# Optimization experiments

Hardware: AMD Instinct MI355X
Metric: run time of the kernel (lower is better)

The kernel has to match this reference:

```python
import jax, jax.numpy as jnp
import numpy as np

M = 41
RHO = M / 2.0          # rho=-1 -> M/2
OVERLAPS = 40
STRIDES = 40
N_FFT = OVERLAPS + STRIDES   # 80
HOP = STRIDES                # 40

def _get_index():
    S = []
    for n1 in range(-(M // 2), M // 2):
        for n2 in range(-(M // 2), M // 2):
            if abs(n1 * n2) <= RHO * (M // 2):
                S.append((n1, n2))
    return np.asarray(S, dtype=np.int64)

IDX = _get_index()          # [K,2], K=1600
N1 = IDX[:, 0]
N2 = IDX[:, 1]
K = len(IDX)

def setup_inputs() -> dict:
    key = jax.random.key(0)
    ks = jax.random.split(key, 7)
    b, L, m = 2, 2080, 2
    return {
        "x_real": jax.random.normal(ks[0], (b, L, m), jnp.float32),
        "x_imag": jax.random.normal(ks[1], (b, L, m), jnp.float32),
        "task_info": jax.random.uniform(ks[2], (b, 4), jnp.float32),
        "w_real": jax.random.normal(ks[3], (K,), jnp.float32) * 0.02,
        "w_imag": jax.random.normal(ks[4], (K,), jnp.float32) * 0.02,
        "b_real": jax.random.normal(ks[5], (1,), jnp.float32) * 0.02,
        "b_imag": jax.random.normal(ks[6], (1,), jnp.float32) * 0.02,
    }

def _stft(x):
    # x: [b, L, m] complex -> [b, T, F, m]; rectangular window, center=False
    L = x.shape[1]
    T = (L - N_FFT) // HOP + 1
    idx = np.arange(T)[:, None] * HOP + np.arange(N_FFT)[None, :]
    frames = x[:, idx, :]                      # [b, T, F, m]
    return jnp.fft.fft(frames, axis=2)

def _istft(X, L):
    # X: [b, T, F, m] -> [b, L, m] via overlap-add, rect-window normalization
    frames = jnp.fft.ifft(X, axis=2)
    b, T, F, m = X.shape
    idx = (np.arange(T)[:, None] * HOP + np.arange(F)[None, :]).reshape(-1)
    y = jnp.zeros((b, L, m), X.dtype).at[:, idx, :].add(frames.reshape(b, -1, m))
    cov = np.zeros(L)
    np.add.at(cov, idx, 1.0)
    cov = jnp.asarray(np.where(cov > 0, cov, 1.0), jnp.float32)
    return y / cov[None, :, None]

def reference(x_real, x_imag, task_info, w_real, w_imag, b_real, b_imag):
    x = x_real + 1j * x_imag                   # [b, L, m] complex64
    b, L, m = x.shape
    # get_power: launch power (dBm in task_info[:,0]) -> mW per mode
    P = jnp.power(10.0, task_info[:, 0] / 10.0) / m   # [b]
    X = _stft(x)                               # [b, T, F, m]
    F = N_FFT
    f = np.arange(F)
    g1 = (f[None, :] - N1[:, None]) % F        # [K, F] : torch.roll(X, n1, dims=2)
    g12 = (f[None, :] - (N1 + N2)[:, None]) % F
    g2 = (f[None, :] - N2[:, None]) % F
    # A_k = roll(X,n1) * conj(roll(X,n1+n2))   -> [b, T, K, F, m]
    A = X[:, :, g1, :] * jnp.conj(X[:, :, g12, :])
    A = A + jnp.roll(A, 1, axis=1)             # + previous frame (circular)
    E = A * X[:, :, g2, :]                     # [b, T, K, F, m]
    w = (w_real + 1j * w_imag).astype(E.dtype)
    bias = (b_real[0] + 1j * b_imag[0]).astype(E.dtype)
    delta = jnp.einsum('btkfm,k->btfm', E, w) + bias   # ComplexLinear(K,1)
    d = _istft(delta, L)                       # [b, L, m]
    out = x + d * P[:, None, None].astype(d.dtype)
    return out[:, OVERLAPS // 2: L - OVERLAPS // 2, :]
```

## Files before the change

kernel.cpp:

```cpp
#include <hip/hip_runtime.h>
#include <math.h>

#define BATCH 2
#define LLEN  2080
#define MCH   2
#define TT    51
#define FF    80
#define HOP   40
#define KW    1600
#define OUTL  2040
#define NT    640
#define NB    (BATCH * TT * MCH)
#define ZROW  161
#define PI_F  3.14159265358979323846f

__global__ __launch_bounds__(NT) void fused_k1(
    const float* __restrict__ xr, const float* __restrict__ xi,
    const float* __restrict__ wr, const float* __restrict__ wi,
    const float* __restrict__ br, const float* __restrict__ bi,
    float2* __restrict__ Fr)
{
    __shared__ float2 xs[2 * FF];
    __shared__ float2 tw[FF];
    __shared__ float2 Yt2[2 * FF];
    __shared__ float2 Yp[FF];
    __shared__ float2 Wsh[KW];
    __shared__ float2 Zall[40][ZROW];
    __shared__ float2 dvec[FF];

    float2* flat = &Zall[0][0];

    int tid = threadIdx.x;
    int bid = blockIdx.x;
    int b   = bid / (TT * MCH);
    int rem = bid % (TT * MCH);
    int t   = rem / MCH;
    int mi  = rem % MCH;
    int tp  = (t + TT - 1) % TT;

    float bre = br[0], bim = bi[0];

    float2 wreg0 = make_float2(wr[tid],        wi[tid]);
    float2 wreg1 = make_float2(wr[tid + NT],   wi[tid + NT]);
    float2 wreg2 = make_float2(0.f, 0.f);
    if (tid < KW - 2 * NT)
        wreg2 = make_float2(wr[tid + 2 * NT], wi[tid + 2 * NT]);

    if (tid < 2 * FF) {
        int frm = tid / FF, j = tid % FF;
        int tt  = (frm == 0) ? t : tp;
        int g = (b * LLEN + tt * HOP + j) * MCH + mi;
        xs[tid] = make_float2(xr[g], xi[g]);
    } else if (tid < 240) {
        int jj = tid - 160;
        float s, c;
        sincosf((2.0f * PI_F / FF) * (float)jj, &s, &c);
        tw[jj] = make_float2(c, s);
    }
    __syncthreads();

    {
        int o    = tid >> 2;
        int pq   = tid & 3;
        int ff   = o % FF;
        int frm  = o / FF;
        const float2* xb = &xs[frm * FF];

        int q = (ff * pq) & 3;
        float2 tv = (q == 0) ? make_float2(1.f, 0.f)
                  : (q == 1) ? make_float2(0.f, -1.f)
                  : (q == 2) ? make_float2(-1.f, 0.f)
                  :            make_float2(0.f, 1.f);
        float sp, cp;
        sincosf(-(2.0f * PI_F / FF) * (float)ff, &sp, &cp);
        float2 st = make_float2(cp, sp);

        float2 a = make_float2(0.f, 0.f);
        int j = pq * 20;
        #pragma unroll 4
        for (int i = 0; i < 20; ++i, ++j) {
            float2 xv = xb[j];
            a.x += xv.x * tv.x - xv.y * tv.y;
            a.y += xv.x * tv.y + xv.y * tv.x;
            float nx = tv.x * st.x - tv.y * st.y;
            tv.y = tv.x * st.y + tv.y * st.x;
            tv.x = nx;
        }
        flat[pq * 160 + o] = a;
    }
    __syncthreads();
    if (tid < 2 * FF) {
        float2 s = make_float2(0.f, 0.f);
        for (int p = 0; p < 4; ++p) {
            float2 v = flat[p * 160 + tid];
            s.x += v.x; s.y += v.y;
        }
        if (tid < FF) {
            Yt2[tid + 20] = s;
            Yt2[(tid < 60) ? (tid + 100) : (tid - 60)] = s;
        } else {
            Yp[tid - FF] = s;
        }
    }
    __syncthreads();

    for (int i = 0; i < 5; ++i) {
        int zi = tid + i * NT;
        int jn = zi / FF;
        int g  = zi % FF;
        int n2 = jn - 20;
        int gm = g - n2; if (gm >= FF) gm -= FF; if (gm < 0) gm += FF;
        float2 a  = Yt2[g + 20], bm = Yt2[gm + 20];
        float2 cc = Yp[g],       dm = Yp[gm];
        float zre = a.x * bm.x + a.y * bm.y + cc.x * dm.x + cc.y * dm.y;
        float zim = a.y * bm.x - a.x * bm.y + cc.y * dm.x - cc.x * dm.y;
        float2 z = make_float2(zre, zim);
        Zall[jn][g + 20] = z;
        Zall[jn][(g < 60) ? (g + 100) : (g - 60)] = z;
    }
    {
        Wsh[tid]      = wreg0;
        Wsh[tid + NT] = wreg1;
        if (tid < KW - 2 * NT) Wsh[tid + 2 * NT] = wreg2;
    }
    __syncthreads();

    float2 o0, o1, o2, o3, o4;
    int jn, fb;
    {
        jn = tid >> 4;
        int fg = tid & 15;
        fb = fg * 5;
        const float2* zz = &Zall[jn][0];

        float2 S0 = make_float2(0.f,0.f), S1 = S0, S2 = S0, S3 = S0, S4 = S0;
        float2 w0 = zz[fb + 40], w1 = zz[fb + 41], w2 = zz[fb + 42],
               w3 = zz[fb + 43], w4 = zz[fb + 44];
        #pragma unroll
        for (int jn1 = 0; jn1 < 40; ++jn1) {
            float2 wv = Wsh[jn1 * 40 + jn];
            S0.x += wv.x * w0.x - wv.y * w0.y;  S0.y += wv.x * w0.y + wv.y * w0.x;
            S1.x += wv.x * w1.x - wv.y * w1.y;  S1.y += wv.x * w1.y + wv.y * w1.x;
            S2.x += wv.x * w2.x - wv.y * w2.y;  S2.y += wv.x * w2.y + wv.y * w2.x;
            S3.x += wv.x * w3.x - wv.y * w3.y;  S3.y += wv.x * w3.y + wv.y * w3.x;
            S4.x += wv.x * w4.x - wv.y * w4.y;  S4.y += wv.x * w4.y + wv.y * w4.x;
            if (jn1 < 39) {
                float2 nv = zz[fb + 39 - jn1];
                w4 = w3; w3 = w2; w2 = w1; w1 = w0; w0 = nv;
            }
        }
        float2 y;
        y = Yt2[fb + 0 - jn + 40]; o0 = make_float2(y.x*S0.x - y.y*S0.y, y.x*S0.y + y.y*S0.x);
        y = Yt2[fb + 1 - jn + 40]; o1 = make_float2(y.x*S1.x - y.y*S1.y, y.x*S1.y + y.y*S1.x);
        y = Yt2[fb + 2 - jn + 40]; o2 = make_float2(y.x*S2.x - y.y*S2.y, y.x*S2.y + y.y*S2.x);
        y = Yt2[fb + 3 - jn + 40]; o3 = make_float2(y.x*S3.x - y.y*S3.y, y.x*S3.y + y.y*S3.x);
        y = Yt2[fb + 4 - jn + 40]; o4 = make_float2(y.x*S4.x - y.y*S4.y, y.x*S4.y + y.y*S4.x);
    }
    __syncthreads();
    flat[jn * FF + fb + 0] = o0;
    flat[jn * FF + fb + 1] = o1;
    flat[jn * FF + fb + 2] = o2;
    flat[jn * FF + fb + 3] = o3;
    flat[jn * FF + fb + 4] = o4;
    __syncthreads();

    {
        int f = tid % FF;
        int p = tid / FF;
        float2 s = make_float2(0.f, 0.f);
        for (int q2 = 0; q2 < 5; ++q2) {
            float2 v = flat[(p * 5 + q2) * FF + f];
            s.x += v.x; s.y += v.y;
        }
        flat[3200 + p * FF + f] = s;
    }
    __syncthreads();
    if (tid < FF) {
        float2 s = make_float2(bre, bim);
        #pragma unroll
        for (int p = 0; p < 8; ++p) {
            float2 v = flat[3200 + p * FF + tid];
            s.x += v.x; s.y += v.y;
        }
        dvec[tid] = s;
    }
    __syncthreads();

    {
        int j  = tid >> 3;
        int p8 = tid & 7;
        float2 a = make_float2(0.f, 0.f);
        int f0 = p8 * 10;
        int r  = (j * f0) % FF;
        #pragma unroll 5
        for (int i = 0; i < 10; ++i) {
            float2 dv = dvec[f0 + i];
            float2 tv = tw[r];
            a.x += dv.x * tv.x - dv.y * tv.y;
            a.y += dv.x * tv.y + dv.y * tv.x;
            r += j; if (r >= FF) r -= FF;
        }
        flat[p8 * FF + j] = a;
    }
    __syncthreads();
    if (tid < FF) {
        float2 s = make_float2(0.f, 0.f);
        #pragma unroll
        for (int p = 0; p < 8; ++p) {
            float2 v = flat[p * FF + tid];
            s.x += v.x; s.y += v.y;
        }
        s.x *= (1.0f / FF);
        s.y *= (1.0f / FF);
        Fr[((b * TT + t) * MCH + mi) * FF + tid] = s;
    }
}

__global__ void out_kernel(
    const float* __restrict__ xr, const float* __restrict__ xi,
    const float* __restrict__ ti, const float2* __restrict__ Fr,
    float* __restrict__ out, int out_size)
{
    int idx = blockIdx.x * blockDim.x + threadIdx.x;
    int tot = BATCH * OUTL * MCH;
    if (idx >= tot) return;
    int mi  = idx % MCH;
    int rem = idx / MCH;
    int lo  = rem % OUTL;
    int b   = rem / OUTL;
    int l   = lo + 20;

    float P = exp2f(ti[b * 4] * 0.33219280948873623f) * 0.5f;

    int t1 = l / HOP;
    int t0 = t1 - 1;
    float2 acc = make_float2(0.f, 0.f);
    float cov = 0.f;
    if (t1 <= TT - 1) {
        float2 v = Fr[((b * TT + t1) * MCH + mi) * FF + (l - HOP * t1)];
        acc.x += v.x; acc.y += v.y; cov += 1.f;
    }
    if (t0 >= 0) {
        float2 v = Fr[((b * TT + t0) * MCH + mi) * FF + (l - HOP * t0)];
        acc.x += v.x; acc.y += v.y; cov += 1.f;
    }
    float inv = 1.0f / cov;
    acc.x *= inv; acc.y *= inv;

    int gi = (b * LLEN + l) * MCH + mi;
    float outr = xr[gi] + acc.x * P;
    if (out_size == tot) {
        out[idx] = outr;
    } else {
        float outi = xi[gi] + acc.y * P;
        out[idx * 2]     = outr;
        out[idx * 2 + 1] = outi;
    }
}

extern "C" void kernel_launch(void* const* d_in, const int* in_sizes, int n_in,
                              void* d_out, int out_size, void* d_ws, size_t ws_size,
                              hipStream_t stream)
{
    const float* xr = (const float*)d_in[0];
    const float* xi = (const float*)d_in[1];
    const float* ti = (const float*)d_in[2];
    const float* wr = (const float*)d_in[3];
    const float* wi = (const float*)d_in[4];
    const float* br = (const float*)d_in[5];
    const float* bi = (const float*)d_in[6];

    float2* Fr = (float2*)d_ws;

    fused_k1<<<NB, NT, 0, stream>>>(xr, xi, wr, wi, br, bi, Fr);

    int tot = BATCH * OUTL * MCH;
    out_kernel<<<(tot + 255) / 256, 256, 0, stream>>>(xr, xi, ti, Fr,
                                                      (float*)d_out, out_size);
}
```

Before: 17.22 us.

## Fuse overlap-add output into single kernel with per-segment duplicate frame work

Merges the two kernels into one. Each block now owns a 40-sample output segment and recomputes both overlapping frames (current and previous), including their DFTs and nonlinear sums, so it can do the overlap-add, normalization and residual write directly. This removes the second launch and the workspace round-trip through global memory. In exchange each block does roughly twice the arithmetic and uses about twice the shared memory, which lowers occupancy. The DFT split is also changed from four partial sums to two, combined with a warp shuffle instead of a shared-memory reduction.

```diff
diff --git a/kernel.cpp b/kernel.cpp
--- a/kernel.cpp
+++ b/kernel.cpp
@@ -10,75 +10,78 @@
 #define KW    1600
 #define OUTL  2040
 #define NT    640
-#define NB    (BATCH * TT * MCH)
+#define NS    52
+#define NB    (BATCH * NS * MCH)
 #define ZROW  161
 #define PI_F  3.14159265358979323846f
 
-__global__ __launch_bounds__(NT) void fused_k1(
+__global__ __launch_bounds__(NT) void mono_kernel(
     const float* __restrict__ xr, const float* __restrict__ xi,
+    const float* __restrict__ ti,
     const float* __restrict__ wr, const float* __restrict__ wi,
     const float* __restrict__ br, const float* __restrict__ bi,
-    float2* __restrict__ Fr)
+    float* __restrict__ out, int out_size)
 {
-    __shared__ float2 xs[2 * FF];
+    __shared__ float2 xs[4 * FF];
     __shared__ float2 tw[FF];
-    __shared__ float2 Yt2[2 * FF];
-    __shared__ float2 Yp[FF];
+    __shared__ float2 Ysh[4][2 * FF];
     __shared__ float2 Wsh[KW];
-    __shared__ float2 Zall[40][ZROW];
-    __shared__ float2 dvec[FF];
-
-    float2* flat = &Zall[0][0];
+    __shared__ float2 Zall[2][40][ZROW];
+    __shared__ float2 dvec[2 * FF];
+
+    float2* flat = &Zall[0][0][0];
 
     int tid = threadIdx.x;
     int bid = blockIdx.x;
-    int b   = bid / (TT * MCH);
-    int rem = bid % (TT * MCH);
-    int t   = rem / MCH;
+    int b   = bid / (NS * MCH);
+    int rem = bid % (NS * MCH);
+    int s   = rem / MCH;
     int mi  = rem % MCH;
-    int tp  = (t + TT - 1) % TT;
+
+    bool dAv = (s <= TT - 1);
+    bool dBv = (s >= 1);
+    int tA  = dAv ? s : 0;
+    int tAp = (tA + TT - 1) % TT;
+    int tB  = dBv ? s - 1 : 0;
+    int tBp = (tB + TT - 1) % TT;
 
     float bre = br[0], bim = bi[0];
 
-    float2 wreg0 = make_float2(wr[tid],        wi[tid]);
-    float2 wreg1 = make_float2(wr[tid + NT],   wi[tid + NT]);
+    float2 wreg0 = make_float2(wr[tid],      wi[tid]);
+    float2 wreg1 = make_float2(wr[tid + NT], wi[tid + NT]);
     float2 wreg2 = make_float2(0.f, 0.f);
     if (tid < KW - 2 * NT)
         wreg2 = make_float2(wr[tid + 2 * NT], wi[tid + 2 * NT]);
 
-    if (tid < 2 * FF) {
-        int frm = tid / FF, j = tid % FF;
-        int tt  = (frm == 0) ? t : tp;
-        int g = (b * LLEN + tt * HOP + j) * MCH + mi;
+    if (tid < 4 * FF) {
+        int slot = tid / FF, j = tid % FF;
+        int tslot = (slot == 0) ? tA : (slot == 1) ? tAp : (slot == 2) ? tB : tBp;
+        int g = (b * LLEN + tslot * HOP + j) * MCH + mi;
         xs[tid] = make_float2(xr[g], xi[g]);
-    } else if (tid < 240) {
-        int jj = tid - 160;
-        float s, c;
-        sincosf((2.0f * PI_F / FF) * (float)jj, &s, &c);
-        tw[jj] = make_float2(c, s);
-    }
-    __syncthreads();
-
-    {
-        int o    = tid >> 2;
-        int pq   = tid & 3;
+    } else if (tid < 4 * FF + FF) {
+        int jj = tid - 4 * FF;
+        float sn, cs;
+        sincosf((2.0f * PI_F / FF) * (float)jj, &sn, &cs);
+        tw[jj] = make_float2(cs, sn);
+    }
+    __syncthreads();
+
+    {
+        int o    = tid >> 1;
+        int pq   = tid & 1;
+        int slot = o / FF;
         int ff   = o % FF;
-        int frm  = o / FF;
-        const float2* xb = &xs[frm * FF];
-
-        int q = (ff * pq) & 3;
-        float2 tv = (q == 0) ? make_float2(1.f, 0.f)
-                  : (q == 1) ? make_float2(0.f, -1.f)
-                  : (q == 2) ? make_float2(-1.f, 0.f)
-                  :            make_float2(0.f, 1.f);
+        const float2* xb = &xs[slot * FF];
+
+        float2 tv = ((ff & pq) & 1) ? make_float2(-1.f, 0.f) : make_float2(1.f, 0.f);
         float sp, cp;
         sincosf(-(2.0f * PI_F / FF) * (float)ff, &sp, &cp);
         float2 st = make_float2(cp, sp);
 
         float2 a = make_float2(0.f, 0.f);
-        int j = pq * 20;
+        int j = pq * 40;
         #pragma unroll 4
-        for (int i = 0; i < 20; ++i, ++j) {
+        for (int i = 0; i < 40; ++i, ++j) {
             float2 xv = xb[j];
             a.x += xv.x * tv.x - xv.y * tv.y;
             a.y += xv.x * tv.y + xv.y * tv.x;
@@ -86,175 +89,161 @@
             tv.y = tv.x * st.y + tv.y * st.x;
             tv.x = nx;
         }
-        flat[pq * 160 + o] = a;
-    }
-    __syncthreads();
-    if (tid < 2 * FF) {
-        float2 s = make_float2(0.f, 0.f);
-        for (int p = 0; p < 4; ++p) {
-            float2 v = flat[p * 160 + tid];
-            s.x += v.x; s.y += v.y;
-        }
-        if (tid < FF) {
-            Yt2[tid + 20] = s;
-            Yt2[(tid < 60) ? (tid + 100) : (tid - 60)] = s;
-        } else {
-            Yp[tid - FF] = s;
-        }
-    }
-    __syncthreads();
-
-    for (int i = 0; i < 5; ++i) {
+        a.x += __shfl_xor(a.x, 1);
+        a.y += __shfl_xor(a.y, 1);
+        if (pq == 0) {
+            Ysh[slot][ff + 20] = a;
+            Ysh[slot][(ff < 60) ? (ff + 100) : (ff - 60)] = a;
+        }
+    }
+    __syncthreads();
+
+    #pragma unroll
+    for (int i = 0; i < 10; ++i) {
         int zi = tid + i * NT;
-        int jn = zi / FF;
-        int g  = zi % FF;
-        int n2 = jn - 20;
-        int gm = g - n2; if (gm >= FF) gm -= FF; if (gm < 0) gm += FF;
-        float2 a  = Yt2[g + 20], bm = Yt2[gm + 20];
-        float2 cc = Yp[g],       dm = Yp[gm];
+        int d  = zi / 3200;
+        int rr = zi % 3200;
+        int jn = rr / FF;
+        int g  = rr % FF;
+        const float2* Ya = Ysh[2 * d];
+        const float2* Yp = Ysh[2 * d + 1];
+        float2 a  = Ya[g + 20], bm = Ya[g - jn + 40];
+        float2 cc = Yp[g + 20], dm = Yp[g - jn + 40];
         float zre = a.x * bm.x + a.y * bm.y + cc.x * dm.x + cc.y * dm.y;
         float zim = a.y * bm.x - a.x * bm.y + cc.y * dm.x - cc.x * dm.y;
         float2 z = make_float2(zre, zim);
-        Zall[jn][g + 20] = z;
-        Zall[jn][(g < 60) ? (g + 100) : (g - 60)] = z;
-    }
-    {
-        Wsh[tid]      = wreg0;
-        Wsh[tid + NT] = wreg1;
-        if (tid < KW - 2 * NT) Wsh[tid + 2 * NT] = wreg2;
-    }
-    __syncthreads();
-
-    float2 o0, o1, o2, o3, o4;
-    int jn, fb;
-    {
-        jn = tid >> 4;
-        int fg = tid & 15;
-        fb = fg * 5;
-        const float2* zz = &Zall[jn][0];
-
-        float2 S0 = make_float2(0.f,0.f), S1 = S0, S2 = S0, S3 = S0, S4 = S0;
-        float2 w0 = zz[fb + 40], w1 = zz[fb + 41], w2 = zz[fb + 42],
-               w3 = zz[fb + 43], w4 = zz[fb + 44];
+        Zall[d][jn][g + 20] = z;
+        Zall[d][jn][(g < 60) ? (g + 100) : (g - 60)] = z;
+    }
+    Wsh[tid]      = wreg0;
+    Wsh[tid + NT] = wreg1;
+    if (tid < KW - 2 * NT) Wsh[tid + 2 * NT] = wreg2;
+    __syncthreads();
+
+    {
+        int d  = tid / 320;
+        int rr = tid % 320;
+        int jn = rr >> 3;
+        int fg = rr & 7;
+        int fb = fg * 10;
+        const float2* zz = &Zall[d][jn][0];
+        const float2* Ya = Ysh[2 * d];
+
+        float2 S[10], W[10];
+        #pragma unroll
+        for (int q = 0; q < 10; ++q) { S[q] = make_float2(0.f, 0.f); W[q] = zz[fb + 40 + q]; }
         #pragma unroll
         for (int jn1 = 0; jn1 < 40; ++jn1) {
             float2 wv = Wsh[jn1 * 40 + jn];
-            S0.x += wv.x * w0.x - wv.y * w0.y;  S0.y += wv.x * w0.y + wv.y * w0.x;
-            S1.x += wv.x * w1.x - wv.y * w1.y;  S1.y += wv.x * w1.y + wv.y * w1.x;
-            S2.x += wv.x * w2.x - wv.y * w2.y;  S2.y += wv.x * w2.y + wv.y * w2.x;
-            S3.x += wv.x * w3.x - wv.y * w3.y;  S3.y += wv.x * w3.y + wv.y * w3.x;
-            S4.x += wv.x * w4.x - wv.y * w4.y;  S4.y += wv.x * w4.y + wv.y * w4.x;
+            #pragma unroll
+            for (int q = 0; q < 10; ++q) {
+                S[q].x += wv.x * W[q].x - wv.y * W[q].y;
+                S[q].y += wv.x * W[q].y + wv.y * W[q].x;
+            }
             if (jn1 < 39) {
-                float2 nv = zz[fb + 39 - jn1];
-                w4 = w3; w3 = w2; w2 = w1; w1 = w0; w0 = nv;
-            }
-        }
-        float2 y;
-        y = Yt2[fb + 0 - jn + 40]; o0 = make_float2(y.x*S0.x - y.y*S0.y, y.x*S0.y + y.y*S0.x);
-        y = Yt2[fb + 1 - jn + 40]; o1 = make_float2(y.x*S1.x - y.y*S1.y, y.x*S1.y + y.y*S1.x);
-        y = Yt2[fb + 2 - jn + 40]; o2 = make_float2(y.x*S2.x - y.y*S2.y, y.x*S2.y + y.y*S2.x);
-        y = Yt2[fb + 3 - jn + 40]; o3 = make_float2(y.x*S3.x - y.y*S3.y, y.x*S3.y + y.y*S3.x);
-        y = Yt2[fb + 4 - jn + 40]; o4 = make_float2(y.x*S4.x - y.y*S4.y, y.x*S4.y + y.y*S4.x);
-    }
-    __syncthreads();
-    flat[jn * FF + fb + 0] = o0;
-    flat[jn * FF + fb + 1] = o1;
-    flat[jn * FF + fb + 2] = o2;
-    flat[jn * FF + fb + 3] = o3;
-    flat[jn * FF + fb + 4] = o4;
-    __syncthreads();
-
-    {
-        int f = tid % FF;
-        int p = tid / FF;
-        float2 s = make_float2(0.f, 0.f);
-        for (int q2 = 0; q2 < 5; ++q2) {
-            float2 v = flat[(p * 5 + q2) * FF + f];
-            s.x += v.x; s.y += v.y;
-        }
-        flat[3200 + p * FF + f] = s;
-    }
-    __syncthreads();
-    if (tid < FF) {
-        float2 s = make_float2(bre, bim);
-        #pragma unroll
-        for (int p = 0; p < 8; ++p) {
-            float2 v = flat[3200 + p * FF + tid];
-            s.x += v.x; s.y += v.y;
-        }
-        dvec[tid] = s;
-    }
-    __syncthreads();
-
-    {
-        int j  = tid >> 3;
-        int p8 = tid & 7;
+                #pragma unroll
+                for (int q = 9; q > 0; --q) W[q] = W[q - 1];
+                W[0] = zz[fb + 39 - jn1];
+            }
+        }
+        float2 O[10];
+        #pragma unroll
+        for (int q = 0; q < 10; ++q) {
+            float2 y = Ya[fb + q - jn + 40];
+            O[q] = make_float2(y.x * S[q].x - y.y * S[q].y,
+                               y.x * S[q].y + y.y * S[q].x);
+        }
+        __syncthreads();
+        #pragma unroll
+        for (int q = 0; q < 10; ++q)
+            flat[d * 3200 + jn * 80 + fb + q] = O[q];
+    }
+    __syncthreads();
+
+    {
+        int d  = tid / 320;
+        int rr = tid % 320;
+        int p  = rr / FF;
+        int f  = rr % FF;
+        float2 sum = make_float2(0.f, 0.f);
+        #pragma unroll
+        for (int q = 0; q < 10; ++q) {
+            float2 v = flat[d * 3200 + (p * 10 + q) * 80 + f];
+            sum.x += v.x; sum.y += v.y;
+        }
+        flat[6400 + d * 320 + p * 80 + f] = sum;
+    }
+    __syncthreads();
+    if (tid < 160) {
+        int d = tid / FF, f = tid % FF;
+        float2 sum = make_float2(bre, bim);
+        #pragma unroll
+        for (int p = 0; p < 4; ++p) {
+            float2 v = flat[6400 + d * 320 + p * 80 + f];
+            sum.x += v.x; sum.y += v.y;
+        }
+        dvec[d * FF + f] = sum;
+    }
+    __syncthreads();
+
+    {
+        int d   = tid / 320;
+        int rr  = tid % 320;
+        int j40 = rr >> 3;
+        int p8  = rr & 7;
+        int j   = j40 + 40 * d;
         float2 a = make_float2(0.f, 0.f);
         int f0 = p8 * 10;
         int r  = (j * f0) % FF;
         #pragma unroll 5
         for (int i = 0; i < 10; ++i) {
-            float2 dv = dvec[f0 + i];
+            float2 dv = dvec[d * FF + f0 + i];
             float2 tv = tw[r];
             a.x += dv.x * tv.x - dv.y * tv.y;
             a.y += dv.x * tv.y + dv.y * tv.x;
             r += j; if (r >= FF) r -= FF;
         }
-        flat[p8 * FF + j] = a;
-    }
-    __syncthreads();
-    if (tid < FF) {
-        float2 s = make_float2(0.f, 0.f);
-        #pragma unroll
-        for (int p = 0; p < 8; ++p) {
-            float2 v = flat[p * FF + tid];
-            s.x += v.x; s.y += v.y;
-        }
-        s.x *= (1.0f / FF);
-        s.y *= (1.0f / FF);
-        Fr[((b * TT + t) * MCH + mi) * FF + tid] = s;
-    }
-}
-
-__global__ void out_kernel(
-    const float* __restrict__ xr, const float* __restrict__ xi,
-    const float* __restrict__ ti, const float2* __restrict__ Fr,
-    float* __restrict__ out, int out_size)
-{
-    int idx = blockIdx.x * blockDim.x + threadIdx.x;
-    int tot = BATCH * OUTL * MCH;
-    if (idx >= tot) return;
-    int mi  = idx % MCH;
-    int rem = idx / MCH;
-    int lo  = rem % OUTL;
-    int b   = rem / OUTL;
-    int l   = lo + 20;
-
-    float P = exp2f(ti[b * 4] * 0.33219280948873623f) * 0.5f;
-
-    int t1 = l / HOP;
-    int t0 = t1 - 1;
-    float2 acc = make_float2(0.f, 0.f);
-    float cov = 0.f;
-    if (t1 <= TT - 1) {
-        float2 v = Fr[((b * TT + t1) * MCH + mi) * FF + (l - HOP * t1)];
-        acc.x += v.x; acc.y += v.y; cov += 1.f;
-    }
-    if (t0 >= 0) {
-        float2 v = Fr[((b * TT + t0) * MCH + mi) * FF + (l - HOP * t0)];
-        acc.x += v.x; acc.y += v.y; cov += 1.f;
-    }
-    float inv = 1.0f / cov;
-    acc.x *= inv; acc.y *= inv;
-
-    int gi = (b * LLEN + l) * MCH + mi;
-    float outr = xr[gi] + acc.x * P;
-    if (out_size == tot) {
-        out[idx] = outr;
-    } else {
-        float outi = xi[gi] + acc.y * P;
-        out[idx * 2]     = outr;
-        out[idx * 2 + 1] = outi;
+        flat[(d * 40 + j40) * 8 + p8] = a;
+    }
+    __syncthreads();
+
+    if (tid < 40) {
+        int j40 = tid;
+        int l = 40 * s + j40;
+        if (l >= 20 && l < LLEN - 20) {
+            float2 acc = make_float2(0.f, 0.f);
+            float cov = 0.f;
+            if (dAv) {
+                #pragma unroll
+                for (int p = 0; p < 8; ++p) {
+                    float2 v = flat[j40 * 8 + p];
+                    acc.x += v.x; acc.y += v.y;
+                }
+                cov += 1.f;
+            }
+            if (dBv) {
+                #pragma unroll
+                for (int p = 0; p < 8; ++p) {
+                    float2 v = flat[(40 + j40) * 8 + p];
+                    acc.x += v.x; acc.y += v.y;
+                }
+                cov += 1.f;
+            }
+            float P   = exp2f(ti[b * 4] * 0.33219280948873623f) * 0.5f;
+            float inv = 1.0f / ((float)FF * cov);
+            float ar = acc.x * inv, ai = acc.y * inv;
+            int gi = (b * LLEN + l) * MCH + mi;
+            int lo = l - 20;
+            int p  = (b * OUTL + lo) * MCH + mi;
+            const int tot = BATCH * OUTL * MCH;
+            float outr = xr[gi] + ar * P;
+            if (out_size == tot) {
+                out[p] = outr;
+            } else {
+                out[p * 2]     = outr;
+                out[p * 2 + 1] = xi[gi] + ai * P;
+            }
+        }
     }
 }
 
@@ -270,11 +259,6 @@
     const float* br = (const float*)d_in[5];
     const float* bi = (const float*)d_in[6];
 
-    float2* Fr = (float2*)d_ws;
-
-    fused_k1<<<NB, NT, 0, stream>>>(xr, xi, wr, wi, br, bi, Fr);
-
-    int tot = BATCH * OUTL * MCH;
-    out_kernel<<<(tot + 255) / 256, 256, 0, stream>>>(xr, xi, ti, Fr,
-                                                      (float*)d_out, out_size);
+    mono_kernel<<<NB, NT, 0, stream>>>(xr, xi, ti, wr, wi, br, bi,
+                                       (float*)d_out, out_size);
 }
```

Result: slower. 21.27 us (+23.5%).

## Split each frame's K-sum across two half-blocks and combine partials in output kernel

Applied to the files above, without the earlier changes.

Each frame/channel block is split into two blocks of 320 threads, each handling half of the n2 index range, which doubles the grid from 204 to 408 blocks and halves shared memory per block. The per-frame DFT now uses a twiddle-table lookup over two partial sums instead of four with on-the-fly rotation. Each half writes its own partial inverse-DFT result to a separate workspace slice, and the output kernel sums the two. The aim is to fill more CUs on the device. In exchange, the forward DFT and the inverse-DFT steps are now computed in both halves, and the output kernel does extra global reads.

```diff
diff --git a/kernel.cpp b/kernel.cpp
--- a/kernel.cpp
+++ b/kernel.cpp
@@ -9,8 +9,9 @@
 #define HOP   40
 #define KW    1600
 #define OUTL  2040
-#define NT    640
-#define NB    (BATCH * TT * MCH)
+#define NT    320
+#define NHB   (BATCH * TT * MCH * 2)
+#define NFR   (BATCH * TT * MCH)
 #define ZROW  161
 #define PI_F  3.14159265358979323846f
 
@@ -18,33 +19,29 @@
     const float* __restrict__ xr, const float* __restrict__ xi,
     const float* __restrict__ wr, const float* __restrict__ wi,
     const float* __restrict__ br, const float* __restrict__ bi,
-    float2* __restrict__ Fr)
+    float2* __restrict__ FrH)
 {
     __shared__ float2 xs[2 * FF];
     __shared__ float2 tw[FF];
     __shared__ float2 Yt2[2 * FF];
     __shared__ float2 Yp[FF];
-    __shared__ float2 Wsh[KW];
-    __shared__ float2 Zall[40][ZROW];
+    __shared__ float2 Wsh[40 * 20];
+    __shared__ float2 Zall[20][ZROW];
     __shared__ float2 dvec[FF];
 
     float2* flat = &Zall[0][0];
 
     int tid = threadIdx.x;
     int bid = blockIdx.x;
-    int b   = bid / (TT * MCH);
-    int rem = bid % (TT * MCH);
+    int h   = bid & 1;
+    int fid = bid >> 1;
+    int b   = fid / (TT * MCH);
+    int rem = fid % (TT * MCH);
     int t   = rem / MCH;
     int mi  = rem % MCH;
     int tp  = (t + TT - 1) % TT;
 
     float bre = br[0], bim = bi[0];
-
-    float2 wreg0 = make_float2(wr[tid],        wi[tid]);
-    float2 wreg1 = make_float2(wr[tid + NT],   wi[tid + NT]);
-    float2 wreg2 = make_float2(0.f, 0.f);
-    if (tid < KW - 2 * NT)
-        wreg2 = make_float2(wr[tid + 2 * NT], wi[tid + 2 * NT]);
 
     if (tid < 2 * FF) {
         int frm = tid / FF, j = tid % FF;
@@ -57,44 +54,36 @@
         sincosf((2.0f * PI_F / FF) * (float)jj, &s, &c);
         tw[jj] = make_float2(c, s);
     }
-    __syncthreads();
-
-    {
-        int o    = tid >> 2;
-        int pq   = tid & 3;
+    for (int k = tid; k < 800; k += NT) {
+        int jn1 = k / 20, jl = k % 20;
+        int src = jn1 * 40 + h * 20 + jl;
+        Wsh[k] = make_float2(wr[src], wi[src]);
+    }
+    __syncthreads();
+
+    {
+        int o    = tid >> 1;
+        int pq   = tid & 1;
         int ff   = o % FF;
         int frm  = o / FF;
         const float2* xb = &xs[frm * FF];
-
-        int q = (ff * pq) & 3;
-        float2 tv = (q == 0) ? make_float2(1.f, 0.f)
-                  : (q == 1) ? make_float2(0.f, -1.f)
-                  : (q == 2) ? make_float2(-1.f, 0.f)
-                  :            make_float2(0.f, 1.f);
-        float sp, cp;
-        sincosf(-(2.0f * PI_F / FF) * (float)ff, &sp, &cp);
-        float2 st = make_float2(cp, sp);
-
         float2 a = make_float2(0.f, 0.f);
-        int j = pq * 20;
-        #pragma unroll 4
-        for (int i = 0; i < 20; ++i, ++j) {
+        int j = pq * 40;
+        int r = (ff * j) % FF;
+        #pragma unroll 5
+        for (int i = 0; i < 40; ++i, ++j) {
             float2 xv = xb[j];
-            a.x += xv.x * tv.x - xv.y * tv.y;
-            a.y += xv.x * tv.y + xv.y * tv.x;
-            float nx = tv.x * st.x - tv.y * st.y;
-            tv.y = tv.x * st.y + tv.y * st.x;
-            tv.x = nx;
+            float2 tv = tw[r];
+            a.x += xv.x * tv.x + xv.y * tv.y;
+            a.y += xv.y * tv.x - xv.x * tv.y;
+            r += ff; if (r >= FF) r -= FF;
         }
         flat[pq * 160 + o] = a;
     }
     __syncthreads();
     if (tid < 2 * FF) {
-        float2 s = make_float2(0.f, 0.f);
-        for (int p = 0; p < 4; ++p) {
-            float2 v = flat[p * 160 + tid];
-            s.x += v.x; s.y += v.y;
-        }
+        float2 v0 = flat[tid], v1 = flat[160 + tid];
+        float2 s = make_float2(v0.x + v1.x, v0.y + v1.y);
         if (tid < FF) {
             Yt2[tid + 20] = s;
             Yt2[(tid < 60) ? (tid + 100) : (tid - 60)] = s;
@@ -106,39 +95,34 @@
 
     for (int i = 0; i < 5; ++i) {
         int zi = tid + i * NT;
-        int jn = zi / FF;
+        int jl = zi / FF;
         int g  = zi % FF;
-        int n2 = jn - 20;
-        int gm = g - n2; if (gm >= FF) gm -= FF; if (gm < 0) gm += FF;
-        float2 a  = Yt2[g + 20], bm = Yt2[gm + 20];
-        float2 cc = Yp[g],       dm = Yp[gm];
+        int n2 = h * 20 + jl - 20;
+        float2 a  = Yt2[g + 20], bm = Yt2[g - n2 + 20];
+        float2 cc = Yp[g],       dm = Yp[(g - n2 + FF) % FF];
         float zre = a.x * bm.x + a.y * bm.y + cc.x * dm.x + cc.y * dm.y;
         float zim = a.y * bm.x - a.x * bm.y + cc.y * dm.x - cc.x * dm.y;
         float2 z = make_float2(zre, zim);
-        Zall[jn][g + 20] = z;
-        Zall[jn][(g < 60) ? (g + 100) : (g - 60)] = z;
-    }
-    {
-        Wsh[tid]      = wreg0;
-        Wsh[tid + NT] = wreg1;
-        if (tid < KW - 2 * NT) Wsh[tid + 2 * NT] = wreg2;
+        Zall[jl][g + 20] = z;
+        Zall[jl][(g < 60) ? (g + 100) : (g - 60)] = z;
     }
     __syncthreads();
 
     float2 o0, o1, o2, o3, o4;
-    int jn, fb;
-    {
-        jn = tid >> 4;
+    int jl, fb;
+    {
+        jl = tid >> 4;
         int fg = tid & 15;
         fb = fg * 5;
-        const float2* zz = &Zall[jn][0];
+        int jn = h * 20 + jl;
+        const float2* zz = &Zall[jl][0];
 
         float2 S0 = make_float2(0.f,0.f), S1 = S0, S2 = S0, S3 = S0, S4 = S0;
         float2 w0 = zz[fb + 40], w1 = zz[fb + 41], w2 = zz[fb + 42],
                w3 = zz[fb + 43], w4 = zz[fb + 44];
         #pragma unroll
         for (int jn1 = 0; jn1 < 40; ++jn1) {
-            float2 wv = Wsh[jn1 * 40 + jn];
+            float2 wv = Wsh[jn1 * 20 + jl];
             S0.x += wv.x * w0.x - wv.y * w0.y;  S0.y += wv.x * w0.y + wv.y * w0.x;
             S1.x += wv.x * w1.x - wv.y * w1.y;  S1.y += wv.x * w1.y + wv.y * w1.x;
             S2.x += wv.x * w2.x - wv.y * w2.y;  S2.y += wv.x * w2.y + wv.y * w2.x;
@@ -157,29 +141,30 @@
         y = Yt2[fb + 4 - jn + 40]; o4 = make_float2(y.x*S4.x - y.y*S4.y, y.x*S4.y + y.y*S4.x);
     }
     __syncthreads();
-    flat[jn * FF + fb + 0] = o0;
-    flat[jn * FF + fb + 1] = o1;
-    flat[jn * FF + fb + 2] = o2;
-    flat[jn * FF + fb + 3] = o3;
-    flat[jn * FF + fb + 4] = o4;
+    flat[jl * FF + fb + 0] = o0;
+    flat[jl * FF + fb + 1] = o1;
+    flat[jl * FF + fb + 2] = o2;
+    flat[jl * FF + fb + 3] = o3;
+    flat[jl * FF + fb + 4] = o4;
     __syncthreads();
 
     {
         int f = tid % FF;
         int p = tid / FF;
         float2 s = make_float2(0.f, 0.f);
+        #pragma unroll
         for (int q2 = 0; q2 < 5; ++q2) {
             float2 v = flat[(p * 5 + q2) * FF + f];
             s.x += v.x; s.y += v.y;
         }
-        flat[3200 + p * FF + f] = s;
+        flat[1600 + p * FF + f] = s;
     }
     __syncthreads();
     if (tid < FF) {
-        float2 s = make_float2(bre, bim);
-        #pragma unroll
-        for (int p = 0; p < 8; ++p) {
-            float2 v = flat[3200 + p * FF + tid];
+        float2 s = (h == 0) ? make_float2(bre, bim) : make_float2(0.f, 0.f);
+        #pragma unroll
+        for (int p = 0; p < 4; ++p) {
+            float2 v = flat[1600 + p * FF + tid];
             s.x += v.x; s.y += v.y;
         }
         dvec[tid] = s;
@@ -187,38 +172,38 @@
     __syncthreads();
 
     {
-        int j  = tid >> 3;
-        int p8 = tid & 7;
+        int j  = tid >> 2;
+        int p4 = tid & 3;
         float2 a = make_float2(0.f, 0.f);
-        int f0 = p8 * 10;
+        int f0 = p4 * 20;
         int r  = (j * f0) % FF;
         #pragma unroll 5
-        for (int i = 0; i < 10; ++i) {
+        for (int i = 0; i < 20; ++i) {
             float2 dv = dvec[f0 + i];
             float2 tv = tw[r];
             a.x += dv.x * tv.x - dv.y * tv.y;
             a.y += dv.x * tv.y + dv.y * tv.x;
             r += j; if (r >= FF) r -= FF;
         }
-        flat[p8 * FF + j] = a;
+        flat[p4 * FF + j] = a;
     }
     __syncthreads();
     if (tid < FF) {
         float2 s = make_float2(0.f, 0.f);
         #pragma unroll
-        for (int p = 0; p < 8; ++p) {
+        for (int p = 0; p < 4; ++p) {
             float2 v = flat[p * FF + tid];
             s.x += v.x; s.y += v.y;
         }
         s.x *= (1.0f / FF);
         s.y *= (1.0f / FF);
-        Fr[((b * TT + t) * MCH + mi) * FF + tid] = s;
+        FrH[(h * NFR + fid) * FF + tid] = s;
     }
 }
 
 __global__ void out_kernel(
     const float* __restrict__ xr, const float* __restrict__ xi,
-    const float* __restrict__ ti, const float2* __restrict__ Fr,
+    const float* __restrict__ ti, const float2* __restrict__ FrH,
     float* __restrict__ out, int out_size)
 {
     int idx = blockIdx.x * blockDim.x + threadIdx.x;
@@ -237,12 +222,16 @@
     float2 acc = make_float2(0.f, 0.f);
     float cov = 0.f;
     if (t1 <= TT - 1) {
-        float2 v = Fr[((b * TT + t1) * MCH + mi) * FF + (l - HOP * t1)];
-        acc.x += v.x; acc.y += v.y; cov += 1.f;
+        int base = ((b * TT + t1) * MCH + mi) * FF + (l - HOP * t1);
+        float2 v0 = FrH[base];
+        float2 v1 = FrH[NFR * FF + base];
+        acc.x += v0.x + v1.x; acc.y += v0.y + v1.y; cov += 1.f;
     }
     if (t0 >= 0) {
-        float2 v = Fr[((b * TT + t0) * MCH + mi) * FF + (l - HOP * t0)];
-        acc.x += v.x; acc.y += v.y; cov += 1.f;
+        int base = ((b * TT + t0) * MCH + mi) * FF + (l - HOP * t0);
+        float2 v0 = FrH[base];
+        float2 v1 = FrH[NFR * FF + base];
+        acc.x += v0.x + v1.x; acc.y += v0.y + v1.y; cov += 1.f;
     }
     float inv = 1.0f / cov;
     acc.x *= inv; acc.y *= inv;
@@ -270,11 +259,11 @@
     const float* br = (const float*)d_in[5];
     const float* bi = (const float*)d_in[6];
 
-    float2* Fr = (float2*)d_ws;
-
-    fused_k1<<<NB, NT, 0, stream>>>(xr, xi, wr, wi, br, bi, Fr);
+    float2* FrH = (float2*)d_ws;
+
+    fused_k1<<<NHB, NT, 0, stream>>>(xr, xi, wr, wi, br, bi, FrH);
 
     int tot = BATCH * OUTL * MCH;
-    out_kernel<<<(tot + 255) / 256, 256, 0, stream>>>(xr, xi, ti, Fr,
+    out_kernel<<<(tot + 255) / 256, 256, 0, stream>>>(xr, xi, ti, FrH,
                                                       (float*)d_out, out_size);
 }
```

Measured after the change: 20.53 us. 19.2% more time.

## Widen fused block to 832 threads, use twiddle table in DFT, separate reduction buffers

Applied to the files above, without the earlier changes.

Raises the fused kernel block size to 832 threads so the main convolution stage runs on 800 threads, each computing 4 frequency outputs instead of 5. The forward DFT now reads twiddles from the shared table instead of a rotating recurrence, and the weights are loaded straight into shared memory. Dedicated shared buffers for the partial sums remove one barrier, and the output kernel uses 64-thread blocks. In exchange there is more shared memory per block, more idle lanes in the other stages, and many more small blocks in the output kernel.

```diff
diff --git a/kernel.cpp b/kernel.cpp
--- a/kernel.cpp
+++ b/kernel.cpp
@@ -9,7 +9,7 @@
 #define HOP   40
 #define KW    1600
 #define OUTL  2040
-#define NT    640
+#define NT    832
 #define NB    (BATCH * TT * MCH)
 #define ZROW  161
 #define PI_F  3.14159265358979323846f
@@ -26,6 +26,8 @@
     __shared__ float2 Yp[FF];
     __shared__ float2 Wsh[KW];
     __shared__ float2 Zall[40][ZROW];
+    __shared__ float2 part3[40][81];
+    __shared__ float2 red2[8][FF];
     __shared__ float2 dvec[FF];
 
     float2* flat = &Zall[0][0];
@@ -39,12 +41,6 @@
     int tp  = (t + TT - 1) % TT;
 
     float bre = br[0], bim = bi[0];
-
-    float2 wreg0 = make_float2(wr[tid],        wi[tid]);
-    float2 wreg1 = make_float2(wr[tid + NT],   wi[tid + NT]);
-    float2 wreg2 = make_float2(0.f, 0.f);
-    if (tid < KW - 2 * NT)
-        wreg2 = make_float2(wr[tid + 2 * NT], wi[tid + 2 * NT]);
 
     if (tid < 2 * FF) {
         int frm = tid / FF, j = tid % FF;
@@ -57,40 +53,33 @@
         sincosf((2.0f * PI_F / FF) * (float)jj, &s, &c);
         tw[jj] = make_float2(c, s);
     }
-    __syncthreads();
-
-    {
+    for (int k = tid; k < KW; k += NT)
+        Wsh[k] = make_float2(wr[k], wi[k]);
+    __syncthreads();
+
+    if (tid < 640) {
         int o    = tid >> 2;
         int pq   = tid & 3;
         int ff   = o % FF;
         int frm  = o / FF;
         const float2* xb = &xs[frm * FF];
-
-        int q = (ff * pq) & 3;
-        float2 tv = (q == 0) ? make_float2(1.f, 0.f)
-                  : (q == 1) ? make_float2(0.f, -1.f)
-                  : (q == 2) ? make_float2(-1.f, 0.f)
-                  :            make_float2(0.f, 1.f);
-        float sp, cp;
-        sincosf(-(2.0f * PI_F / FF) * (float)ff, &sp, &cp);
-        float2 st = make_float2(cp, sp);
-
         float2 a = make_float2(0.f, 0.f);
         int j = pq * 20;
-        #pragma unroll 4
+        int r = (ff * j) % FF;
+        #pragma unroll 5
         for (int i = 0; i < 20; ++i, ++j) {
             float2 xv = xb[j];
-            a.x += xv.x * tv.x - xv.y * tv.y;
-            a.y += xv.x * tv.y + xv.y * tv.x;
-            float nx = tv.x * st.x - tv.y * st.y;
-            tv.y = tv.x * st.y + tv.y * st.x;
-            tv.x = nx;
+            float2 tv = tw[r];
+            a.x += xv.x * tv.x + xv.y * tv.y;
+            a.y += xv.y * tv.x - xv.x * tv.y;
+            r += ff; if (r >= FF) r -= FF;
         }
         flat[pq * 160 + o] = a;
     }
     __syncthreads();
     if (tid < 2 * FF) {
         float2 s = make_float2(0.f, 0.f);
+        #pragma unroll
         for (int p = 0; p < 4; ++p) {
             float2 v = flat[p * 160 + tid];
             s.x += v.x; s.y += v.y;
@@ -104,8 +93,7 @@
     }
     __syncthreads();
 
-    for (int i = 0; i < 5; ++i) {
-        int zi = tid + i * NT;
+    for (int zi = tid; zi < 3200; zi += NT) {
         int jn = zi / FF;
         int g  = zi % FF;
         int n2 = jn - 20;
@@ -118,24 +106,16 @@
         Zall[jn][g + 20] = z;
         Zall[jn][(g < 60) ? (g + 100) : (g - 60)] = z;
     }
-    {
-        Wsh[tid]      = wreg0;
-        Wsh[tid + NT] = wreg1;
-        if (tid < KW - 2 * NT) Wsh[tid + 2 * NT] = wreg2;
-    }
-    __syncthreads();
-
-    float2 o0, o1, o2, o3, o4;
-    int jn, fb;
-    {
-        jn = tid >> 4;
-        int fg = tid & 15;
-        fb = fg * 5;
+    __syncthreads();
+
+    if (tid < 800) {
+        int jn = tid % 40;
+        int fg = tid / 40;
+        int fb = fg * 4;
         const float2* zz = &Zall[jn][0];
 
-        float2 S0 = make_float2(0.f,0.f), S1 = S0, S2 = S0, S3 = S0, S4 = S0;
-        float2 w0 = zz[fb + 40], w1 = zz[fb + 41], w2 = zz[fb + 42],
-               w3 = zz[fb + 43], w4 = zz[fb + 44];
+        float2 S0 = make_float2(0.f,0.f), S1 = S0, S2 = S0, S3 = S0;
+        float2 w0 = zz[fb + 40], w1 = zz[fb + 41], w2 = zz[fb + 42], w3 = zz[fb + 43];
         #pragma unroll
         for (int jn1 = 0; jn1 < 40; ++jn1) {
             float2 wv = Wsh[jn1 * 40 + jn];
@@ -143,50 +123,47 @@
             S1.x += wv.x * w1.x - wv.y * w1.y;  S1.y += wv.x * w1.y + wv.y * w1.x;
             S2.x += wv.x * w2.x - wv.y * w2.y;  S2.y += wv.x * w2.y + wv.y * w2.x;
             S3.x += wv.x * w3.x - wv.y * w3.y;  S3.y += wv.x * w3.y + wv.y * w3.x;
-            S4.x += wv.x * w4.x - wv.y * w4.y;  S4.y += wv.x * w4.y + wv.y * w4.x;
             if (jn1 < 39) {
                 float2 nv = zz[fb + 39 - jn1];
-                w4 = w3; w3 = w2; w2 = w1; w1 = w0; w0 = nv;
+                w3 = w2; w2 = w1; w1 = w0; w0 = nv;
             }
         }
         float2 y;
-        y = Yt2[fb + 0 - jn + 40]; o0 = make_float2(y.x*S0.x - y.y*S0.y, y.x*S0.y + y.y*S0.x);
-        y = Yt2[fb + 1 - jn + 40]; o1 = make_float2(y.x*S1.x - y.y*S1.y, y.x*S1.y + y.y*S1.x);
-        y = Yt2[fb + 2 - jn + 40]; o2 = make_float2(y.x*S2.x - y.y*S2.y, y.x*S2.y + y.y*S2.x);
-        y = Yt2[fb + 3 - jn + 40]; o3 = make_float2(y.x*S3.x - y.y*S3.y, y.x*S3.y + y.y*S3.x);
-        y = Yt2[fb + 4 - jn + 40]; o4 = make_float2(y.x*S4.x - y.y*S4.y, y.x*S4.y + y.y*S4.x);
-    }
-    __syncthreads();
-    flat[jn * FF + fb + 0] = o0;
-    flat[jn * FF + fb + 1] = o1;
-    flat[jn * FF + fb + 2] = o2;
-    flat[jn * FF + fb + 3] = o3;
-    flat[jn * FF + fb + 4] = o4;
-    __syncthreads();
-
-    {
+        y = Yt2[fb + 0 - jn + 40];
+        part3[jn][fb + 0] = make_float2(y.x*S0.x - y.y*S0.y, y.x*S0.y + y.y*S0.x);
+        y = Yt2[fb + 1 - jn + 40];
+        part3[jn][fb + 1] = make_float2(y.x*S1.x - y.y*S1.y, y.x*S1.y + y.y*S1.x);
+        y = Yt2[fb + 2 - jn + 40];
+        part3[jn][fb + 2] = make_float2(y.x*S2.x - y.y*S2.y, y.x*S2.y + y.y*S2.x);
+        y = Yt2[fb + 3 - jn + 40];
+        part3[jn][fb + 3] = make_float2(y.x*S3.x - y.y*S3.y, y.x*S3.y + y.y*S3.x);
+    }
+    __syncthreads();
+
+    if (tid < 640) {
         int f = tid % FF;
         int p = tid / FF;
         float2 s = make_float2(0.f, 0.f);
+        #pragma unroll
         for (int q2 = 0; q2 < 5; ++q2) {
-            float2 v = flat[(p * 5 + q2) * FF + f];
-            s.x += v.x; s.y += v.y;
-        }
-        flat[3200 + p * FF + f] = s;
+            float2 v = part3[p * 5 + q2][f];
+            s.x += v.x; s.y += v.y;
+        }
+        red2[p][f] = s;
     }
     __syncthreads();
     if (tid < FF) {
         float2 s = make_float2(bre, bim);
         #pragma unroll
         for (int p = 0; p < 8; ++p) {
-            float2 v = flat[3200 + p * FF + tid];
+            float2 v = red2[p][tid];
             s.x += v.x; s.y += v.y;
         }
         dvec[tid] = s;
     }
     __syncthreads();
 
-    {
+    if (tid < 640) {
         int j  = tid >> 3;
         int p8 = tid & 7;
         float2 a = make_float2(0.f, 0.f);
@@ -200,14 +177,14 @@
             a.y += dv.x * tv.y + dv.y * tv.x;
             r += j; if (r >= FF) r -= FF;
         }
-        flat[p8 * FF + j] = a;
+        red2[p8][j] = a;
     }
     __syncthreads();
     if (tid < FF) {
         float2 s = make_float2(0.f, 0.f);
         #pragma unroll
         for (int p = 0; p < 8; ++p) {
-            float2 v = flat[p * FF + tid];
+            float2 v = red2[p][tid];
             s.x += v.x; s.y += v.y;
         }
         s.x *= (1.0f / FF);
@@ -216,12 +193,12 @@
     }
 }
 
-__global__ void out_kernel(
+__global__ __launch_bounds__(64) void out_kernel(
     const float* __restrict__ xr, const float* __restrict__ xi,
     const float* __restrict__ ti, const float2* __restrict__ Fr,
     float* __restrict__ out, int out_size)
 {
-    int idx = blockIdx.x * blockDim.x + threadIdx.x;
+    int idx = blockIdx.x * 64 + threadIdx.x;
     int tot = BATCH * OUTL * MCH;
     if (idx >= tot) return;
     int mi  = idx % MCH;
@@ -275,6 +252,6 @@
     fused_k1<<<NB, NT, 0, stream>>>(xr, xi, wr, wi, br, bi, Fr);
 
     int tot = BATCH * OUTL * MCH;
-    out_kernel<<<(tot + 255) / 256, 256, 0, stream>>>(xr, xi, ti, Fr,
-                                                      (float*)d_out, out_size);
+    out_kernel<<<(tot + 63) / 64, 64, 0, stream>>>(xr, xi, ti, Fr,
+                                                   (float*)d_out, out_size);
 }
```

New measurement: 17.97 us. 4.4% more time.
